# Kernel tuning notes

Hardware: AMD Instinct MI355X
Metric: run time of the kernel (lower is better)

The kernel has to match this reference:

```python
import jax, jax.numpy as jnp
import numpy as np
import math

N, E, H, A = 50000, 800000, 128, 8
D = H // A


def setup_inputs() -> dict:
    key = jax.random.key(0)
    ks = jax.random.split(key, 12)
    q = jax.random.normal(ks[0], (N, H), dtype=jnp.float32)
    k = jax.random.normal(ks[1], (N, H), dtype=jnp.float32)
    v = jax.random.normal(ks[2], (N, H), dtype=jnp.float32)
    Wq = jax.random.normal(ks[3], (H, H), dtype=jnp.float32) * 0.05
    bq = jax.random.normal(ks[4], (H,), dtype=jnp.float32) * 0.05
    Wk = jax.random.normal(ks[5], (H, H), dtype=jnp.float32) * 0.05
    bk = jax.random.normal(ks[6], (H,), dtype=jnp.float32) * 0.05
    Wv = jax.random.normal(ks[7], (H, H), dtype=jnp.float32) * 0.05
    bv = jax.random.normal(ks[8], (H,), dtype=jnp.float32) * 0.05
    # Ensure every node id appears at least once in q_indices so that
    # q_indices.unique() == arange(N) and the output shape is static [N, H].
    tail = jax.random.randint(ks[9], (E - N,), 0, N)
    q_indices = jnp.concatenate([jnp.arange(N), tail]).astype(jnp.int32)
    k_indices = jax.random.randint(ks[10], (E,), 0, N).astype(jnp.int32)
    return {"q": q, "k": k, "v": v, "Wq": Wq, "bq": bq, "Wk": Wk, "bk": bk,
            "Wv": Wv, "bv": bv, "q_indices": q_indices, "k_indices": k_indices}


def reference(q, k, v, Wq, bq, Wk, bk, Wv, bv, q_indices, k_indices):
    n = q.shape[0]
    # Gather node features per edge (irregular access).
    qe = q[q_indices]            # [E, H]
    ke = k[k_indices]            # [E, H]
    ve = v[k_indices]            # [E, H]
    # Linear projections (torch Linear: x @ W.T + b), split heads -> [E, A, D].
    Q = (qe @ Wq.T + bq).reshape(-1, A, D)
    K = (ke @ Wk.T + bk).reshape(-1, A, D)
    V = (ve @ Wv.T + bv).reshape(-1, A, D)
    # Per-edge scaled dot-product scores: [E, A].
    scores = jnp.einsum('ead,ead->ea', Q, K) / math.sqrt(D)
    # Segment softmax over edges sharing the same destination node
    # (faithful to the original: plain exp, no max subtraction).
    ex = jnp.exp(scores)                                        # [E, A]
    denom = jax.ops.segment_sum(ex, q_indices, num_segments=n)  # [N, A]
    probs = ex / denom[q_indices]                               # [E, A]
    # Scatter-aggregate weighted values per destination node: [N, A, D].
    ctx = jax.ops.segment_sum(probs[:, :, None] * V, q_indices, num_segments=n)
    # Merge heads -> [N, H].
    return ctx.reshape(n, A * D)
```

## Files before the change

kernel.cpp:

```cpp
#include <hip/hip_runtime.h>
#include <hip/hip_bf16.h>

#define HDIM 128
#define ISTR 136
#define OSTR 264

typedef __attribute__((ext_vector_type(8))) short bf16x8;
typedef __attribute__((ext_vector_type(4))) float f32x4;

__device__ inline unsigned short f2bf(float f) {
    return __builtin_bit_cast(unsigned short, __float2bfloat16(f));
}
__device__ inline float bflo(unsigned u) { return __uint_as_float(u << 16); }
__device__ inline float bfhi(unsigned u) { return __uint_as_float(u & 0xffff0000u); }

__global__ void init_kernel(int* __restrict__ deg, int n,
                            const float* __restrict__ Wq, const float* __restrict__ Wk,
                            const float* __restrict__ Wv, unsigned short* __restrict__ Wopt) {
    int i = blockIdx.x * 256 + threadIdx.x;
    if (i < n) deg[i] = 0;
    if (i < 3 * HDIM * HDIM) {
        int j  = i & 7;
        int l  = (i >> 3) & 63;
        int ks = (i >> 9) & 3;
        int nt = (i >> 11) & 7;
        int m  = i >> 14;
        const float* W = (m == 0) ? Wq : (m == 1) ? Wk : Wv;
        int row = nt * 16 + (l & 15);
        int col = ks * 32 + ((l >> 4) << 3) + j;
        Wopt[i] = f2bf(W[row * HDIM + col]);
    }
}

__global__ void proj_deg(const float* __restrict__ qin, const float* __restrict__ kin,
                         const float* __restrict__ vin, const unsigned short* __restrict__ Wopt,
                         const float* __restrict__ bq, const float* __restrict__ bk,
                         const float* __restrict__ bv,
                         unsigned short* __restrict__ Qb, unsigned short* __restrict__ KVb,
                         const int* __restrict__ qidx, int* __restrict__ deg,
                         int* __restrict__ rank, int E, int n, int nbx, int ndeg, int ntot)
{
    __shared__ unsigned short tile[64 * ISTR];

    const int id     = blockIdx.x;
    const int before = (int)(((long)id * ndeg) / ntot);
    const bool isdeg = (int)(((long)(id + 1) * ndeg) / ntot) > before;

    if (isdeg) {
        const int e0 = before * 1024 + (int)threadIdx.x * 4;
        if (e0 + 4 <= E) {
            const int4 qi = *(const int4*)&qidx[e0];
            int4 r;
            r.x = atomicAdd(&deg[qi.x], 1);
            r.y = atomicAdd(&deg[qi.y], 1);
            r.z = atomicAdd(&deg[qi.z], 1);
            r.w = atomicAdd(&deg[qi.w], 1);
            *(int4*)&rank[e0] = r;
        } else {
            #pragma unroll
            for (int j = 0; j < 4; ++j)
                if (e0 + j < E) rank[e0 + j] = atomicAdd(&deg[qidx[e0 + j]], 1);
        }
        return;
    }

    const int pid = id - before;
    const bool isQ = (pid < nbx);
    const int bx  = isQ ? pid : (pid - nbx);

    const int tid  = threadIdx.x;
    const int lane = tid & 63;
    const int wv   = tid >> 6;
    const int r15  = lane & 15;
    const int quad = lane >> 4;
    const long node0 = (long)bx * 64;
    const int srow = tid >> 5;
    const int sc4  = tid & 31;

    bf16x8 af[4];

#define STAGE_REGS(dst)                                                        \
    {                                                                          \
        _Pragma("unroll")                                                      \
        for (int it = 0; it < 8; ++it) {                                       \
            int row = srow + it * 8;                                           \
            float4 val = dst[it];                                              \
            ushort4 h;                                                         \
            h.x = f2bf(val.x); h.y = f2bf(val.y);                              \
            h.z = f2bf(val.z); h.w = f2bf(val.w);                              \
            *(ushort4*)&tile[row * ISTR + sc4 * 4] = h;                        \
        }                                                                      \
    }

#define LOAD_FRAGS()                                                           \
    {                                                                          \
        _Pragma("unroll")                                                      \
        for (int ks = 0; ks < 4; ++ks)                                         \
            af[ks] = *(const bf16x8*)&tile[(wv * 16 + r15) * ISTR + quad * 8 + ks * 32]; \
    }

#define MFMA_ALL(Wm, acc)                                                      \
    {                                                                          \
        _Pragma("unroll")                                                      \
        for (int nt = 0; nt < 8; ++nt) {                                       \
            acc[nt] = (f32x4){0.f, 0.f, 0.f, 0.f};                             \
            _Pragma("unroll")                                                  \
            for (int ks = 0; ks < 4; ++ks) {                                   \
                const bf16x8 wfrag =                                           \
                    *(const bf16x8*)((Wm) + ((size_t)((nt * 4 + ks) * 64) + lane) * 8); \
                acc[nt] = __builtin_amdgcn_mfma_f32_16x16x32_bf16(af[ks], wfrag, acc[nt], 0, 0, 0); \
            }                                                                  \
        }                                                                      \
    }

    if (isQ) {
        #pragma unroll
        for (int it = 0; it < 8; ++it) {
            int row = srow + it * 8;
            long node = node0 + row;
            float4 val = make_float4(0.f, 0.f, 0.f, 0.f);
            if (node < n) val = ((const float4*)(qin + node * HDIM))[sc4];
            ushort4 h;
            h.x = f2bf(val.x); h.y = f2bf(val.y); h.z = f2bf(val.z); h.w = f2bf(val.w);
            *(ushort4*)&tile[row * ISTR + sc4 * 4] = h;
        }
        __syncthreads();

        f32x4 acc[8];
        LOAD_FRAGS();
        MFMA_ALL(Wopt, acc);
        __syncthreads();

        #pragma unroll
        for (int nt = 0; nt < 8; ++nt) {
            const int c = nt * 16 + r15;
            const float bias = bq[c];
            #pragma unroll
            for (int r = 0; r < 4; ++r)
                tile[(wv * 16 + quad * 4 + r) * ISTR + c] = f2bf(acc[nt][r] + bias);
        }
        __syncthreads();

        #pragma unroll
        for (int it = 0; it < 4; ++it) {
            int g   = it * 256 + tid;
            int row = g >> 4;
            int col = (g & 15) * 8;
            long node = node0 + row;
            if (node < n) {
                ushort4 lo = *(const ushort4*)&tile[row * ISTR + col];
                ushort4 hi = *(const ushort4*)&tile[row * ISTR + col + 4];
                uint4 o;
                o.x = (unsigned)lo.x | ((unsigned)lo.y << 16);
                o.y = (unsigned)lo.z | ((unsigned)lo.w << 16);
                o.z = (unsigned)hi.x | ((unsigned)hi.y << 16);
                o.w = (unsigned)hi.z | ((unsigned)hi.w << 16);
                *(uint4*)&Qb[node * HDIM + col] = o;
            }
        }
    } else {
        float4 kreg[8], vreg[8];
        #pragma unroll
        for (int it = 0; it < 8; ++it) {
            long node = node0 + srow + it * 8;
            if (node < n) {
                kreg[it] = ((const float4*)(kin + node * HDIM))[sc4];
                vreg[it] = ((const float4*)(vin + node * HDIM))[sc4];
            } else {
                kreg[it] = make_float4(0.f, 0.f, 0.f, 0.f);
                vreg[it] = make_float4(0.f, 0.f, 0.f, 0.f);
            }
        }

        f32x4 accK[8], accV[8];

        STAGE_REGS(kreg);
        __syncthreads();
        LOAD_FRAGS();
        MFMA_ALL(Wopt + HDIM * HDIM, accK);
        __syncthreads();

        STAGE_REGS(vreg);
        __syncthreads();
        LOAD_FRAGS();
        MFMA_ALL(Wopt + 2 * HDIM * HDIM, accV);
        __syncthreads();

        #pragma unroll
        for (int h = 0; h < 2; ++h) {
            if ((wv >> 1) == h) {
                #pragma unroll
                for (int nt = 0; nt < 8; ++nt) {
                    const int c = nt * 16 + r15;
                    const float bK = bk[c], bV = bv[c];
                    const int slot = (c >> 2) * 8 + 2 * (c & 3);
                    #pragma unroll
                    for (int r = 0; r < 4; ++r) {
                        const int lr = (wv & 1) * 16 + quad * 4 + r;
                        unsigned pk = (unsigned)f2bf(accK[nt][r] + bK)
                                    | ((unsigned)f2bf(accV[nt][r] + bV) << 16);
                        *(unsigned*)&tile[lr * OSTR + slot] = pk;
                    }
                }
            }
            __syncthreads();
            #pragma unroll
            for (int it = 0; it < 4; ++it) {
                int g   = it * 256 + tid;
                int row = g >> 5;
                int ch  = g & 31;
                long node = node0 + h * 32 + row;
                if (node < n)
                    *(uint4*)&KVb[(size_t)node * 256 + ch * 8] =
                        *(const uint4*)&tile[row * OSTR + ch * 8];
            }
            __syncthreads();
        }
    }
#undef STAGE_REGS
#undef LOAD_FRAGS
#undef MFMA_ALL
}

__global__ void scan_block(const int* __restrict__ deg, int* __restrict__ offs,
                           int* __restrict__ bsum, int n) {
    __shared__ int ws[17];
    const int tid = threadIdx.x;
    const int lane = tid & 63, wv = tid >> 6;
    int i = blockIdx.x * 1024 + tid;
    int v = (i < n) ? deg[i] : 0;
    int sc = v;
    #pragma unroll
    for (int d = 1; d < 64; d <<= 1) {
        int t = __shfl_up(sc, d, 64);
        if (lane >= d) sc += t;
    }
    if (lane == 63) ws[wv] = sc;
    __syncthreads();
    if (tid == 0) {
        int base = 0;
        #pragma unroll
        for (int w = 0; w < 16; ++w) { int t = ws[w]; ws[w] = base; base += t; }
        ws[16] = base;
    }
    __syncthreads();
    if (i < n) offs[i] = ws[wv] + (sc - v);
    if (tid == 0) bsum[blockIdx.x] = ws[16];
}

__global__ void scan_addtops(const int* __restrict__ bsum, int* __restrict__ offs,
                             int n, int E, int nb) {
    __shared__ int s_base;
    const int tid = threadIdx.x;
    if (tid < 64) {
        int v = (tid < nb) ? bsum[tid] : 0;
        int sc = v;
        #pragma unroll
        for (int d = 1; d < 64; d <<= 1) {
            int t = __shfl_up(sc, d, 64);
            if (tid >= d) sc += t;
        }
        if (tid == blockIdx.x) s_base = sc - v;
    }
    __syncthreads();
    int i = blockIdx.x * 1024 + tid;
    if (i < n) offs[i] += s_base;
    if (blockIdx.x == 0 && tid == 0) offs[n] = E;
}

__global__ void fill_kernel(const int* __restrict__ qidx, const int* __restrict__ kidx,
                            const int* __restrict__ offs, const int* __restrict__ rank,
                            int* __restrict__ srcl, int E) {
    int e0 = (blockIdx.x * 256 + (int)threadIdx.x) * 4;
    if (e0 + 4 <= E) {
        const int4 qi = *(const int4*)&qidx[e0];
        const int4 ki = *(const int4*)&kidx[e0];
        const int4 rk = *(const int4*)&rank[e0];
        srcl[offs[qi.x] + rk.x] = ki.x;
        srcl[offs[qi.y] + rk.y] = ki.y;
        srcl[offs[qi.z] + rk.z] = ki.z;
        srcl[offs[qi.w] + rk.w] = ki.w;
    } else {
        #pragma unroll
        for (int j = 0; j < 4; ++j)
            if (e0 + j < E) srcl[offs[qidx[e0 + j]] + rank[e0 + j]] = kidx[e0 + j];
    }
}

__global__ void agg_kernel(const uint2* __restrict__ Q2, const uint4* __restrict__ KV4,
                           const int* __restrict__ offs, const int* __restrict__ srcl,
                           float* __restrict__ out, int n)
{
    const int tid  = threadIdx.x;
    const int l32  = tid & 31;
    const int node = blockIdx.x * 8 + (tid >> 5);
    if (node >= n) return;

    const uint2 qp = Q2[(size_t)node * 32 + l32];
    const float qx = bflo(qp.x), qy = bfhi(qp.x), qz = bflo(qp.y), qw = bfhi(qp.y);

    float dsum = 0.f, a0 = 0.f, a1 = 0.f, a2 = 0.f, a3 = 0.f;
    const int beg = offs[node], end = offs[node + 1];
    const int srcbase = tid & 32;

#define EDGE_STEP(kv)                                                          \
    {                                                                          \
        float part = qx * bflo((kv).x) + qy * bflo((kv).y)                     \
                   + qz * bflo((kv).z) + qw * bflo((kv).w);                    \
        part += __shfl_xor(part, 1, 64);                                       \
        part += __shfl_xor(part, 2, 64);                                       \
        float w = __expf(part * 0.25f);                                        \
        dsum += w;                                                             \
        a0 += w * bfhi((kv).x); a1 += w * bfhi((kv).y);                        \
        a2 += w * bfhi((kv).z); a3 += w * bfhi((kv).w);                        \
    }

    for (int base = beg; base < end; base += 32) {
        int cnt = min(32, end - base);
        int my = (base + l32 < end) ? srcl[base + l32] : 0;
        int j = 0;
        for (; j + 4 <= cnt; j += 4) {
            int s0 = __shfl(my, srcbase + j,     64);
            int s1 = __shfl(my, srcbase + j + 1, 64);
            int s2 = __shfl(my, srcbase + j + 2, 64);
            int s3 = __shfl(my, srcbase + j + 3, 64);
            uint4 kv0 = KV4[(size_t)s0 * 32 + l32];
            uint4 kv1 = KV4[(size_t)s1 * 32 + l32];
            uint4 kv2 = KV4[(size_t)s2 * 32 + l32];
            uint4 kv3 = KV4[(size_t)s3 * 32 + l32];
            EDGE_STEP(kv0); EDGE_STEP(kv1); EDGE_STEP(kv2); EDGE_STEP(kv3);
        }
        for (; j < cnt; ++j) {
            int s = __shfl(my, srcbase + j, 64);
            uint4 kv = KV4[(size_t)s * 32 + l32];
            EDGE_STEP(kv);
        }
    }
#undef EDGE_STEP

    float inv = 1.f / dsum;
    float4 r = make_float4(a0 * inv, a1 * inv, a2 * inv, a3 * inv);
    *(float4*)&out[(size_t)node * HDIM + l32 * 4] = r;
}

extern "C" void kernel_launch(void* const* d_in, const int* in_sizes, int n_in,
                              void* d_out, int out_size, void* d_ws, size_t ws_size,
                              hipStream_t stream) {
    const float* q  = (const float*)d_in[0];
    const float* k  = (const float*)d_in[1];
    const float* v  = (const float*)d_in[2];
    const float* Wq = (const float*)d_in[3];
    const float* bq = (const float*)d_in[4];
    const float* Wk = (const float*)d_in[5];
    const float* bk = (const float*)d_in[6];
    const float* Wv = (const float*)d_in[7];
    const float* bv = (const float*)d_in[8];
    const int* qidx = (const int*)d_in[9];
    const int* kidx = (const int*)d_in[10];
    float* out = (float*)d_out;

    const int N = in_sizes[0] / HDIM;
    const int E = in_sizes[9];

    char* p = (char*)d_ws;
    unsigned short* Qb  = (unsigned short*)p; p += (size_t)N * HDIM * sizeof(unsigned short);
    unsigned short* KVb = (unsigned short*)p; p += (size_t)2 * N * HDIM * sizeof(unsigned short);
    unsigned short* Wopt = (unsigned short*)p; p += (size_t)3 * HDIM * HDIM * sizeof(unsigned short);
    int* deg  = (int*)p; p += (size_t)N * sizeof(int);
    int* offs = (int*)p; p += (size_t)(N + 1) * sizeof(int);
    int* bsum = (int*)p; p += 64 * sizeof(int);
    int* rank = (int*)p; p += (size_t)E * sizeof(int);
    int* srcl = (int*)p; p += (size_t)E * sizeof(int);

    const int nbx  = (N + 63) / 64;
    const int ndeg = (E + 1023) / 1024;
    const int ntot = 2 * nbx + ndeg;
    const int nfb  = (E + 1023) / 1024;
    const int nb   = (N + 1023) / 1024;
    const int initn = (N > 3 * HDIM * HDIM) ? N : 3 * HDIM * HDIM;

    init_kernel<<<(initn + 255) / 256, 256, 0, stream>>>(deg, N, Wq, Wk, Wv, Wopt);
    proj_deg<<<ntot, 256, 0, stream>>>(q, k, v, Wopt, bq, bk, bv, Qb, KVb,
                                       qidx, deg, rank, E, N, nbx, ndeg, ntot);
    scan_block<<<nb, 1024, 0, stream>>>(deg, offs, bsum, N);
    scan_addtops<<<nb, 1024, 0, stream>>>(bsum, offs, N, E, nb);
    fill_kernel<<<nfb, 256, 0, stream>>>(qidx, kidx, offs, rank, srcl, E);
    agg_kernel<<<(N + 7) / 8, 256, 0, stream>>>((const uint2*)Qb, (const uint4*)KVb,
                                                offs, srcl, out, N);
}
```

Baseline: 243.5 us.

## Defer block-prefix add into consumers and software-pipeline edge gathers in aggregation

The second scan pass, which rewrote every offset, is replaced by a single tiny kernel that computes only the per-block prefixes. Fill and aggregation now add the block prefix on the fly, which saves a full pass over the offsets array. The aggregation loop drops the shuffle-based index broadcast, reads srcl directly, and prefetches the next four KV rows while the current four are processed, with masked weights for padding edges. Stores into srcl use nontemporal hints. The trade-offs are extra bpre loads, redundant per-lane srcl reads, and wasted loads on padded tail edges.

```diff
diff --git a/kernel.cpp b/kernel.cpp
--- a/kernel.cpp
+++ b/kernel.cpp
@@ -244,52 +244,46 @@
         ws[16] = base;
     }
     __syncthreads();
-    if (i < n) offs[i] = ws[wv] + (sc - v);
+    if (i <= n) offs[i] = ws[wv] + (sc - v);
     if (tid == 0) bsum[blockIdx.x] = ws[16];
 }
 
-__global__ void scan_addtops(const int* __restrict__ bsum, int* __restrict__ offs,
-                             int n, int E, int nb) {
-    __shared__ int s_base;
+__global__ void scan_tops(const int* __restrict__ bsum, int* __restrict__ bpre, int nb) {
     const int tid = threadIdx.x;
-    if (tid < 64) {
-        int v = (tid < nb) ? bsum[tid] : 0;
-        int sc = v;
-        #pragma unroll
-        for (int d = 1; d < 64; d <<= 1) {
-            int t = __shfl_up(sc, d, 64);
-            if (tid >= d) sc += t;
-        }
-        if (tid == blockIdx.x) s_base = sc - v;
-    }
-    __syncthreads();
-    int i = blockIdx.x * 1024 + tid;
-    if (i < n) offs[i] += s_base;
-    if (blockIdx.x == 0 && tid == 0) offs[n] = E;
+    int v = (tid < nb) ? bsum[tid] : 0;
+    int sc = v;
+    #pragma unroll
+    for (int d = 1; d < 64; d <<= 1) {
+        int t = __shfl_up(sc, d, 64);
+        if (tid >= d) sc += t;
+    }
+    if (tid < nb) bpre[tid] = sc - v;
 }
 
 __global__ void fill_kernel(const int* __restrict__ qidx, const int* __restrict__ kidx,
-                            const int* __restrict__ offs, const int* __restrict__ rank,
-                            int* __restrict__ srcl, int E) {
+                            const int* __restrict__ offs, const int* __restrict__ bpre,
+                            const int* __restrict__ rank, int* __restrict__ srcl, int E) {
     int e0 = (blockIdx.x * 256 + (int)threadIdx.x) * 4;
     if (e0 + 4 <= E) {
         const int4 qi = *(const int4*)&qidx[e0];
         const int4 ki = *(const int4*)&kidx[e0];
         const int4 rk = *(const int4*)&rank[e0];
-        srcl[offs[qi.x] + rk.x] = ki.x;
-        srcl[offs[qi.y] + rk.y] = ki.y;
-        srcl[offs[qi.z] + rk.z] = ki.z;
-        srcl[offs[qi.w] + rk.w] = ki.w;
+        __builtin_nontemporal_store(ki.x, &srcl[offs[qi.x] + bpre[qi.x >> 10] + rk.x]);
+        __builtin_nontemporal_store(ki.y, &srcl[offs[qi.y] + bpre[qi.y >> 10] + rk.y]);
+        __builtin_nontemporal_store(ki.z, &srcl[offs[qi.z] + bpre[qi.z >> 10] + rk.z]);
+        __builtin_nontemporal_store(ki.w, &srcl[offs[qi.w] + bpre[qi.w >> 10] + rk.w]);
     } else {
         #pragma unroll
         for (int j = 0; j < 4; ++j)
-            if (e0 + j < E) srcl[offs[qidx[e0 + j]] + rank[e0 + j]] = kidx[e0 + j];
+            if (e0 + j < E)
+                __builtin_nontemporal_store(kidx[e0 + j],
+                    &srcl[offs[qidx[e0 + j]] + bpre[qidx[e0 + j] >> 10] + rank[e0 + j]]);
     }
 }
 
 __global__ void agg_kernel(const uint2* __restrict__ Q2, const uint4* __restrict__ KV4,
-                           const int* __restrict__ offs, const int* __restrict__ srcl,
-                           float* __restrict__ out, int n)
+                           const int* __restrict__ offs, const int* __restrict__ bpre,
+                           const int* __restrict__ srcl, float* __restrict__ out, int n)
 {
     const int tid  = threadIdx.x;
     const int l32  = tid & 31;
@@ -299,44 +293,40 @@
     const uint2 qp = Q2[(size_t)node * 32 + l32];
     const float qx = bflo(qp.x), qy = bfhi(qp.x), qz = bflo(qp.y), qw = bfhi(qp.y);
 
+    const int beg = offs[node]     + bpre[node >> 10];
+    const int end = offs[node + 1] + bpre[(node + 1) >> 10];
+    const int cnt = end - beg;
+    const int iters = (cnt + 3) >> 2;
+
     float dsum = 0.f, a0 = 0.f, a1 = 0.f, a2 = 0.f, a3 = 0.f;
-    const int beg = offs[node], end = offs[node + 1];
-    const int srcbase = tid & 32;
-
-#define EDGE_STEP(kv)                                                          \
+
+#define LD(j) (KV4[(size_t)srcl[beg + min((j), cnt - 1)] * 32 + l32])
+
+#define STEP(kv, idx)                                                          \
     {                                                                          \
         float part = qx * bflo((kv).x) + qy * bflo((kv).y)                     \
                    + qz * bflo((kv).z) + qw * bflo((kv).w);                    \
         part += __shfl_xor(part, 1, 64);                                       \
         part += __shfl_xor(part, 2, 64);                                       \
-        float w = __expf(part * 0.25f);                                        \
+        float w = ((idx) < cnt) ? __expf(part * 0.25f) : 0.f;                  \
         dsum += w;                                                             \
         a0 += w * bfhi((kv).x); a1 += w * bfhi((kv).y);                        \
         a2 += w * bfhi((kv).z); a3 += w * bfhi((kv).w);                        \
     }
 
-    for (int base = beg; base < end; base += 32) {
-        int cnt = min(32, end - base);
-        int my = (base + l32 < end) ? srcl[base + l32] : 0;
-        int j = 0;
-        for (; j + 4 <= cnt; j += 4) {
-            int s0 = __shfl(my, srcbase + j,     64);
-            int s1 = __shfl(my, srcbase + j + 1, 64);
-            int s2 = __shfl(my, srcbase + j + 2, 64);
-            int s3 = __shfl(my, srcbase + j + 3, 64);
-            uint4 kv0 = KV4[(size_t)s0 * 32 + l32];
-            uint4 kv1 = KV4[(size_t)s1 * 32 + l32];
-            uint4 kv2 = KV4[(size_t)s2 * 32 + l32];
-            uint4 kv3 = KV4[(size_t)s3 * 32 + l32];
-            EDGE_STEP(kv0); EDGE_STEP(kv1); EDGE_STEP(kv2); EDGE_STEP(kv3);
-        }
-        for (; j < cnt; ++j) {
-            int s = __shfl(my, srcbase + j, 64);
-            uint4 kv = KV4[(size_t)s * 32 + l32];
-            EDGE_STEP(kv);
-        }
-    }
-#undef EDGE_STEP
+    uint4 c0 = LD(0), c1 = LD(1), c2 = LD(2), c3 = LD(3);
+    for (int g = 0; g < iters; ++g) {
+        uint4 n0 = {0, 0, 0, 0}, n1 = {0, 0, 0, 0}, n2 = {0, 0, 0, 0}, n3 = {0, 0, 0, 0};
+        const int nb4 = (g + 1) * 4;
+        if (g + 1 < iters) {
+            n0 = LD(nb4); n1 = LD(nb4 + 1); n2 = LD(nb4 + 2); n3 = LD(nb4 + 3);
+        }
+        const int base = g * 4;
+        STEP(c0, base); STEP(c1, base + 1); STEP(c2, base + 2); STEP(c3, base + 3);
+        c0 = n0; c1 = n1; c2 = n2; c3 = n3;
+    }
+#undef LD
+#undef STEP
 
     float inv = 1.f / dsum;
     float4 r = make_float4(a0 * inv, a1 * inv, a2 * inv, a3 * inv);
@@ -369,6 +359,7 @@
     int* deg  = (int*)p; p += (size_t)N * sizeof(int);
     int* offs = (int*)p; p += (size_t)(N + 1) * sizeof(int);
     int* bsum = (int*)p; p += 64 * sizeof(int);
+    int* bpre = (int*)p; p += 64 * sizeof(int);
     int* rank = (int*)p; p += (size_t)E * sizeof(int);
     int* srcl = (int*)p; p += (size_t)E * sizeof(int);
 
@@ -376,15 +367,15 @@
     const int ndeg = (E + 1023) / 1024;
     const int ntot = 2 * nbx + ndeg;
     const int nfb  = (E + 1023) / 1024;
-    const int nb   = (N + 1023) / 1024;
+    const int nb   = (N + 1024) / 1024;
     const int initn = (N > 3 * HDIM * HDIM) ? N : 3 * HDIM * HDIM;
 
     init_kernel<<<(initn + 255) / 256, 256, 0, stream>>>(deg, N, Wq, Wk, Wv, Wopt);
     proj_deg<<<ntot, 256, 0, stream>>>(q, k, v, Wopt, bq, bk, bv, Qb, KVb,
                                        qidx, deg, rank, E, N, nbx, ndeg, ntot);
     scan_block<<<nb, 1024, 0, stream>>>(deg, offs, bsum, N);
-    scan_addtops<<<nb, 1024, 0, stream>>>(bsum, offs, N, E, nb);
-    fill_kernel<<<nfb, 256, 0, stream>>>(qidx, kidx, offs, rank, srcl, E);
+    scan_tops<<<1, 64, 0, stream>>>(bsum, bpre, nb);
+    fill_kernel<<<nfb, 256, 0, stream>>>(qidx, kidx, offs, bpre, rank, srcl, E);
     agg_kernel<<<(N + 7) / 8, 256, 0, stream>>>((const uint2*)Qb, (const uint4*)KVb,
-                                                offs, srcl, out, N);
-}
+                                                offs, bpre, srcl, out, N);
+}
```

Measured after the change: 255.3 us. 1.05x slower.
